# Kernel tuning notes

Hardware: AMD Instinct MI355X
Metric: run time of the kernel (lower is better)

Reference implementation:

```python
import jax, jax.numpy as jnp
import numpy as np
from jax import lax

WIN_SIZE = 11
SIGMA = 1.5
CHANNELS = 3
C1 = (0.01 * 255) ** 2
C2 = (0.03 * 255) ** 2


def fspecial_gauss(size, sigma, channels):
    x, y = np.mgrid[-size // 2 + 1:size // 2 + 1, -size // 2 + 1:size // 2 + 1]
    g = np.exp(-((x ** 2 + y ** 2) / (2.0 * sigma ** 2)))
    g = (g / g.sum()).astype(np.float32)
    # depthwise kernel, OIHW with I=1, O=channels
    return jnp.asarray(np.tile(g[None, None], (channels, 1, 1, 1)))


def _gauss_filter(x, win):
    # depthwise valid conv, NCHW
    return lax.conv_general_dilated(
        x, win, window_strides=(1, 1), padding='VALID',
        feature_group_count=x.shape[1],
        dimension_numbers=('NCHW', 'OIHW', 'NCHW'))


def setup_inputs() -> dict:
    key = jax.random.key(0)
    k1, k2 = jax.random.split(key)
    X = jax.random.uniform(k1, (32, 3, 512, 512), dtype=jnp.float32)
    Y = jax.random.uniform(k2, (32, 3, 512, 512), dtype=jnp.float32)
    win = fspecial_gauss(WIN_SIZE, SIGMA, CHANNELS)
    return {"X": X, "Y": Y, "win": win}


def reference(X, Y, win):
    mu1 = _gauss_filter(X, win)
    mu2 = _gauss_filter(Y, win)
    mu1_sq = mu1 * mu1
    mu2_sq = mu2 * mu2
    mu1_mu2 = mu1 * mu2
    sigma1_sq = _gauss_filter(X * X, win) - mu1_sq
    sigma2_sq = _gauss_filter(Y * Y, win) - mu2_sq
    sigma12 = _gauss_filter(X * Y, win) - mu1_mu2
    cs_map = jax.nn.relu((2 * sigma12 + C2) / (sigma1_sq + sigma2_sq + C2))
    ssim_map = (2 * mu1_mu2 + C1) / (mu1_sq + mu2_sq + C1) * cs_map
    ssim_val = jnp.mean(ssim_map, axis=(1, 2, 3))  # per-image SSIM
    return 1.0 - jnp.mean(ssim_val)  # as_loss=True
```

## Files before the change

### kernel.cpp

```cpp
#include <hip/hip_runtime.h>
#include <math.h>


#define WIN   11
#define IMG   512
#define OUT_N 502
#define TO_R  32
#define TO_C  64
#define TI_R  (TO_R + WIN - 1)
#define TI_C  (TO_C + WIN - 1)
#define VB_W  76
#define C1F   6.5025f
#define C2F   58.5225f

struct GaussW { float w[WIN]; };

__global__ __launch_bounds__(256) void ssim_v2_kernel(
    const float* __restrict__ X, const float* __restrict__ Y,
    GaussW gw, double* __restrict__ acc)
{
    __shared__ float vb[5][TO_R][VB_W];

    const int plane = blockIdx.z;
    const int ox0 = blockIdx.x * TO_C;
    const int oy0 = blockIdx.y * TO_R;
    const float* Xp = X + (size_t)plane * IMG * IMG;
    const float* Yp = Y + (size_t)plane * IMG * IMG;
    const int tid = threadIdx.x;

    for (int item = tid; item < 4 * TI_C; item += 256) {
        const int s = item / TI_C;
        const int c = item - s * TI_C;
        int gc = ox0 + c; if (gc > IMG - 1) gc = IMG - 1;
        const int r0 = oy0 + s * 8;

        float a0[8] = {0}, a1[8] = {0}, a2[8] = {0}, a3[8] = {0}, a4[8] = {0};
#pragma unroll
        for (int k = 0; k < 18; ++k) {
            int gr = r0 + k; if (gr > IMG - 1) gr = IMG - 1;
            size_t off = (size_t)gr * IMG + gc;
            float x = Xp[off];
            float y = Yp[off];
            float xx = x * x, yy = y * y, xy = x * y;
            const int jlo = (k > 10) ? (k - 10) : 0;
            const int jhi = (k < 7) ? k : 7;
#pragma unroll
            for (int j = jlo; j <= jhi; ++j) {
                float wv = gw.w[k - j];
                a0[j] += wv * x;
                a1[j] += wv * y;
                a2[j] += wv * xx;
                a3[j] += wv * yy;
                a4[j] += wv * xy;
            }
        }
#pragma unroll
        for (int j = 0; j < 8; ++j) {
            int i = s * 8 + j;
            vb[0][i][c] = a0[j];
            vb[1][i][c] = a1[j];
            vb[2][i][c] = a2[j];
            vb[3][i][c] = a3[j];
            vb[4][i][c] = a4[j];
        }
    }
    __syncthreads();

    const int i  = tid >> 3;
    const int c0 = (tid & 7) * 8;
    float m[5][8];
#pragma unroll
    for (int f = 0; f < 5; ++f) {
        float v[20];
        const float4* p = (const float4*)&vb[f][i][c0];
#pragma unroll
        for (int q = 0; q < 5; ++q) {
            float4 t = p[q];
            v[4 * q + 0] = t.x; v[4 * q + 1] = t.y;
            v[4 * q + 2] = t.z; v[4 * q + 3] = t.w;
        }
#pragma unroll
        for (int j = 0; j < 8; ++j) {
            float s = 0.f;
#pragma unroll
            for (int k = 0; k < WIN; ++k) s += gw.w[k] * v[j + k];
            m[f][j] = s;
        }
    }

    float psum = 0.f;
    const int gi = oy0 + i;
#pragma unroll
    for (int j = 0; j < 8; ++j) {
        int gj = ox0 + c0 + j;
        if (gi < OUT_N && gj < OUT_N) {
            float m1 = m[0][j], m2 = m[1][j];
            float mu1s = m1 * m1, mu2s = m2 * m2, mu12 = m1 * m2;
            float sig1 = m[2][j] - mu1s;
            float sig2 = m[3][j] - mu2s;
            float sig12 = m[4][j] - mu12;
            float cs = (2.f * sig12 + C2F) / (sig1 + sig2 + C2F);
            cs = fmaxf(cs, 0.f);
            psum += (2.f * mu12 + C1F) / (mu1s + mu2s + C1F) * cs;
        }
    }

#pragma unroll
    for (int off = 32; off > 0; off >>= 1)
        psum += __shfl_down(psum, off, 64);
    __shared__ float wsum[4];
    if ((tid & 63) == 0) wsum[tid >> 6] = psum;
    __syncthreads();
    if (tid == 0) {
        float s = wsum[0] + wsum[1] + wsum[2] + wsum[3];
        atomicAdd(acc, (double)s);
    }
}

__global__ void ssim_finalize_kernel(const double* __restrict__ acc,
                                     float* __restrict__ out)
{
    if (threadIdx.x == 0 && blockIdx.x == 0) {
        const double count = (double)96 * OUT_N * OUT_N;
        out[0] = (float)(1.0 - (*acc) / count);
    }
}

extern "C" void kernel_launch(void* const* d_in, const int* in_sizes, int n_in,
                              void* d_out, int out_size, void* d_ws, size_t ws_size,
                              hipStream_t stream) {
    (void)in_sizes; (void)n_in; (void)out_size; (void)ws_size;
    const float* X = (const float*)d_in[0];
    const float* Y = (const float*)d_in[1];
    float* out = (float*)d_out;
    double* acc = (double*)d_ws;

    hipMemsetAsync(d_ws, 0, sizeof(double), stream);

    GaussW gw;
    {
        double g[WIN], s = 0.0;
        for (int i = 0; i < WIN; ++i) {
            double d = (double)(i - 5);
            g[i] = exp(-(d * d) / (2.0 * 1.5 * 1.5));
            s += g[i];
        }
        for (int i = 0; i < WIN; ++i) gw.w[i] = (float)(g[i] / s);
    }

    dim3 grid((OUT_N + TO_C - 1) / TO_C,
              (OUT_N + TO_R - 1) / TO_R,
              96);
    ssim_v2_kernel<<<grid, 256, 0, stream>>>(X, Y, gw, acc);
    ssim_finalize_kernel<<<1, 64, 0, stream>>>(acc, out);
}
```

Baseline: 314.8 us.

## Retile SSIM to 54-wide output tiles and fuse finalize into last block

Changes the tile so the 64-column input halo exactly matches the 256 threads, which removes the strided loop where only part of the block worked on the second iteration of the vertical pass. The horizontal pass now has each thread compute 4 outputs over two row passes, and launch bounds request 4 blocks per CU. The separate finalize kernel is replaced by a last-block-done counter with a threadfence, saving one launch. In exchange the grid grows from 8x16 to 10x16 blocks per plane, so more halo rows are reloaded and some lanes in the horizontal pass compute outputs that are then discarded.

Measured after the change: 634.9 us. 2.02x slower.

```diff
diff --git a/kernel.cpp b/kernel.cpp
--- a/kernel.cpp
+++ b/kernel.cpp
@@ -5,21 +5,24 @@
 #define WIN   11
 #define IMG   512
 #define OUT_N 502
+#define TO_C  54
 #define TO_R  32
-#define TO_C  64
-#define TI_R  (TO_R + WIN - 1)
-#define TI_C  (TO_C + WIN - 1)
-#define VB_W  76
+#define TI_C  64
+#define GX    10
+#define GY    16
+#define NBLK  (GX * GY * 96)
 #define C1F   6.5025f
 #define C2F   58.5225f
 
 struct GaussW { float w[WIN]; };
 
-__global__ __launch_bounds__(256) void ssim_v2_kernel(
+__global__ __launch_bounds__(256, 4) void ssim_v3_kernel(
     const float* __restrict__ X, const float* __restrict__ Y,
-    GaussW gw, double* __restrict__ acc)
+    GaussW gw, double* __restrict__ acc, unsigned* __restrict__ cnt,
+    float* __restrict__ out)
 {
-    __shared__ float vb[5][TO_R][VB_W];
+    __shared__ float vb[5][TO_R][TI_C];
+    __shared__ float wsum[4];
 
     const int plane = blockIdx.z;
     const int ox0 = blockIdx.x * TO_C;
@@ -28,13 +31,18 @@
     const float* Yp = Y + (size_t)plane * IMG * IMG;
     const int tid = threadIdx.x;
 
-    for (int item = tid; item < 4 * TI_C; item += 256) {
-        const int s = item / TI_C;
-        const int c = item - s * TI_C;
+    {
+        const int c = tid & 63;
+        const int s = tid >> 6;
         int gc = ox0 + c; if (gc > IMG - 1) gc = IMG - 1;
         const int r0 = oy0 + s * 8;
 
-        float a0[8] = {0}, a1[8] = {0}, a2[8] = {0}, a3[8] = {0}, a4[8] = {0};
+        float a[5][8];
+#pragma unroll
+        for (int f = 0; f < 5; ++f)
+#pragma unroll
+            for (int j = 0; j < 8; ++j) a[f][j] = 0.f;
+
 #pragma unroll
         for (int k = 0; k < 18; ++k) {
             int gr = r0 + k; if (gr > IMG - 1) gr = IMG - 1;
@@ -47,82 +55,81 @@
 #pragma unroll
             for (int j = jlo; j <= jhi; ++j) {
                 float wv = gw.w[k - j];
-                a0[j] += wv * x;
-                a1[j] += wv * y;
-                a2[j] += wv * xx;
-                a3[j] += wv * yy;
-                a4[j] += wv * xy;
+                a[0][j] += wv * x;
+                a[1][j] += wv * y;
+                a[2][j] += wv * xx;
+                a[3][j] += wv * yy;
+                a[4][j] += wv * xy;
             }
         }
 #pragma unroll
-        for (int j = 0; j < 8; ++j) {
-            int i = s * 8 + j;
-            vb[0][i][c] = a0[j];
-            vb[1][i][c] = a1[j];
-            vb[2][i][c] = a2[j];
-            vb[3][i][c] = a3[j];
-            vb[4][i][c] = a4[j];
-        }
+        for (int f = 0; f < 5; ++f)
+#pragma unroll
+            for (int j = 0; j < 8; ++j)
+                vb[f][s * 8 + j][c] = a[f][j];
     }
     __syncthreads();
 
-    const int i  = tid >> 3;
-    const int c0 = (tid & 7) * 8;
-    float m[5][8];
+    const int t  = tid & 15;
+    const int i0 = tid >> 4;
+    const int c0 = 4 * t;
+    float psum = 0.f;
+
 #pragma unroll
-    for (int f = 0; f < 5; ++f) {
-        float v[20];
-        const float4* p = (const float4*)&vb[f][i][c0];
+    for (int pass = 0; pass < 2; ++pass) {
+        const int i = i0 + 16 * pass;
+        const int gi = oy0 + i;
+        float m[5][4];
 #pragma unroll
-        for (int q = 0; q < 5; ++q) {
-            float4 t = p[q];
-            v[4 * q + 0] = t.x; v[4 * q + 1] = t.y;
-            v[4 * q + 2] = t.z; v[4 * q + 3] = t.w;
+        for (int f = 0; f < 5; ++f) {
+            float v[16];
+#pragma unroll
+            for (int q = 0; q < 4; ++q) {
+                int cq = c0 + 4 * q; if (cq > 60) cq = 60;
+                float4 tt = *(const float4*)&vb[f][i][cq];
+                v[4 * q + 0] = tt.x; v[4 * q + 1] = tt.y;
+                v[4 * q + 2] = tt.z; v[4 * q + 3] = tt.w;
+            }
+#pragma unroll
+            for (int oc = 0; oc < 4; ++oc) {
+                float s = 0.f;
+#pragma unroll
+                for (int k = 0; k < WIN; ++k) s += gw.w[k] * v[oc + k];
+                m[f][oc] = s;
+            }
         }
 #pragma unroll
-        for (int j = 0; j < 8; ++j) {
-            float s = 0.f;
-#pragma unroll
-            for (int k = 0; k < WIN; ++k) s += gw.w[k] * v[j + k];
-            m[f][j] = s;
-        }
-    }
-
-    float psum = 0.f;
-    const int gi = oy0 + i;
-#pragma unroll
-    for (int j = 0; j < 8; ++j) {
-        int gj = ox0 + c0 + j;
-        if (gi < OUT_N && gj < OUT_N) {
-            float m1 = m[0][j], m2 = m[1][j];
-            float mu1s = m1 * m1, mu2s = m2 * m2, mu12 = m1 * m2;
-            float sig1 = m[2][j] - mu1s;
-            float sig2 = m[3][j] - mu2s;
-            float sig12 = m[4][j] - mu12;
-            float cs = (2.f * sig12 + C2F) / (sig1 + sig2 + C2F);
-            cs = fmaxf(cs, 0.f);
-            psum += (2.f * mu12 + C1F) / (mu1s + mu2s + C1F) * cs;
+        for (int oc = 0; oc < 4; ++oc) {
+            int lc = c0 + oc;
+            int gj = ox0 + lc;
+            if (lc < TO_C && gi < OUT_N && gj < OUT_N) {
+                float m1 = m[0][oc], m2 = m[1][oc];
+                float mu1s = m1 * m1, mu2s = m2 * m2, mu12 = m1 * m2;
+                float sig1 = m[2][oc] - mu1s;
+                float sig2 = m[3][oc] - mu2s;
+                float sig12 = m[4][oc] - mu12;
+                float cs = (2.f * sig12 + C2F) / (sig1 + sig2 + C2F);
+                cs = fmaxf(cs, 0.f);
+                psum += (2.f * mu12 + C1F) / (mu1s + mu2s + C1F) * cs;
+            }
         }
     }
 
 #pragma unroll
     for (int off = 32; off > 0; off >>= 1)
         psum += __shfl_down(psum, off, 64);
-    __shared__ float wsum[4];
     if ((tid & 63) == 0) wsum[tid >> 6] = psum;
     __syncthreads();
     if (tid == 0) {
         float s = wsum[0] + wsum[1] + wsum[2] + wsum[3];
         atomicAdd(acc, (double)s);
-    }
-}
-
-__global__ void ssim_finalize_kernel(const double* __restrict__ acc,
-                                     float* __restrict__ out)
-{
-    if (threadIdx.x == 0 && blockIdx.x == 0) {
-        const double count = (double)96 * OUT_N * OUT_N;
-        out[0] = (float)(1.0 - (*acc) / count);
+        __threadfence();
+        unsigned done = atomicAdd(cnt, 1u);
+        if (done == NBLK - 1) {
+            double tot = atomicAdd(acc, 0.0);
+            const double count = (double)96 * OUT_N * OUT_N;
+            out[0] = (float)(1.0 - tot / count);
+        }
     }
 }
 
@@ -134,8 +141,9 @@
     const float* Y = (const float*)d_in[1];
     float* out = (float*)d_out;
     double* acc = (double*)d_ws;
+    unsigned* cnt = (unsigned*)((char*)d_ws + 8);
 
-    hipMemsetAsync(d_ws, 0, sizeof(double), stream);
+    hipMemsetAsync(d_ws, 0, 16, stream);
 
     GaussW gw;
     {
@@ -148,9 +156,6 @@
         for (int i = 0; i < WIN; ++i) gw.w[i] = (float)(g[i] / s);
     }
 
-    dim3 grid((OUT_N + TO_C - 1) / TO_C,
-              (OUT_N + TO_R - 1) / TO_R,
-              96);
-    ssim_v2_kernel<<<grid, 256, 0, stream>>>(X, Y, gw, acc);
-    ssim_finalize_kernel<<<1, 64, 0, stream>>>(acc, out);
+    dim3 grid(GX, GY, 96);
+    ssim_v3_kernel<<<grid, 256, 0, stream>>>(X, Y, gw, acc, cnt, out);
 }
```
